# Kernel tuning notes

Hardware: AMD Instinct MI355X
Metric: run time of the kernel (lower is better)

## Reference

```python
import jax, jax.numpy as jnp
import numpy as np

N_NODES = 50000


def setup_inputs() -> dict:
    key = jax.random.key(0)
    ks = jax.random.split(key, 9)
    x = jax.random.normal(ks[0], (N_NODES, 32), dtype=jnp.float32)
    pos = jax.random.normal(ks[1], (N_NODES, 3), dtype=jnp.float32)
    edge_index = jax.random.randint(ks[2], (2, 1600000), 0, N_NODES, dtype=jnp.int64)
    W1 = jax.random.normal(ks[3], (35, 64), dtype=jnp.float32) * 0.1
    b1 = jnp.zeros((64,), dtype=jnp.float32)
    W2 = jax.random.normal(ks[4], (64, 64), dtype=jnp.float32) * 0.1
    b2 = jnp.zeros((64,), dtype=jnp.float32)
    Wg = jax.random.normal(ks[5], (64, 128), dtype=jnp.float32) * 0.1
    bg = jnp.zeros((128,), dtype=jnp.float32)
    return {"x": x, "pos": pos, "edge_index": edge_index,
            "W1": W1, "b1": b1, "W2": W2, "b2": b2, "Wg": Wg, "bg": bg}


def reference(x, pos, edge_index, W1, b1, W2, b2, Wg, bg):
    N = x.shape[0]
    # add_self_loops=True: append (i, i) edges
    self_idx = jnp.arange(N, dtype=edge_index.dtype)
    src = jnp.concatenate([edge_index[0], self_idx])  # message source j
    dst = jnp.concatenate([edge_index[1], self_idx])  # aggregation target i
    # message: concat(x_j, pos_j - pos_i) -> local_nn (Lin+ReLU x2)
    msg = jnp.concatenate([x[src], pos[src] - pos[dst]], axis=-1)  # [E+N, 35]
    h = jax.nn.relu(msg @ W1 + b1)  # [E+N, 64]
    h = jax.nn.relu(h @ W2 + b2)    # [E+N, 64]
    # max aggregation per destination node (self loops guarantee nonempty segments)
    agg = jax.ops.segment_max(h, dst, num_segments=N)  # [N, 64]
    # global_nn: Linear
    return agg @ Wg + bg  # [N, 128]
```

## Files before the change

kernel.cpp:

```cpp
#include <hip/hip_runtime.h>

#define N_NODES 50000
#define N_EDGES 1600000
#define N_TOTAL (N_EDGES + N_NODES)
#define F_IN    32
#define HID     64
#define F_OUT   128
#define G       32
#define NB      1563
#define NBIN    392
#define CAP1_MAX 5120
#define OVF_CAP 16384
#define W1WIN   4096
#define NNODEBLK 196

#define OFF_QBF   0
#define OFF_CUR1  (N_NODES * 32)
#define OFF_OVFC  (OFF_CUR1 + NBIN * 16)
#define OFF_CELLB (OFF_OVFC + 16)
#define OFF_CELLC (OFF_CELLB + NB)
#define OFF_OVF   (OFF_CELLC + NB + 2)
#define OFF_BIN   (OFF_OVF + OVF_CAP)
#define NCLR      (NBIN * 16 + 16)

typedef __attribute__((ext_vector_type(2))) _Float16 h2f;
typedef __attribute__((ext_vector_type(8))) _Float16 half8;
typedef __attribute__((ext_vector_type(4))) float v4f;

__device__ __forceinline__ unsigned f2h2(float a, float b) {
    h2f v;
    v.x = (_Float16)a; v.y = (_Float16)b;
    return __builtin_bit_cast(unsigned, v);
}

__device__ __forceinline__ unsigned hsubmax0(unsigned a, unsigned b) {
    h2f x = __builtin_bit_cast(h2f, a) - __builtin_bit_cast(h2f, b);
    h2f z = {(_Float16)0.f, (_Float16)0.f};
    x = __builtin_elementwise_max(x, z);
    return __builtin_bit_cast(unsigned, x);
}

__device__ __forceinline__ float h2lo(unsigned u) { return (float)__builtin_bit_cast(h2f, u).x; }
__device__ __forceinline__ float h2hi(unsigned u) { return (float)__builtin_bit_cast(h2f, u).y; }
__device__ __forceinline__ float f16r(float x)    { return (float)(_Float16)x; }

#define WAVE_FENCE() do { asm volatile("s_waitcnt lgkmcnt(0)" ::: "memory"); \
                          __builtin_amdgcn_sched_barrier(0); } while (0)

__global__ __launch_bounds__(256) void zero_kernel(unsigned* __restrict__ clr)
{
    const int i = blockIdx.x * 256 + threadIdx.x;
    if (i < NCLR) clr[i] = 0u;
}

__global__ __launch_bounds__(1024) void bin_kernel(
    const int* __restrict__ ei, unsigned* __restrict__ cur1,
    unsigned* __restrict__ bin1, unsigned* __restrict__ ovfc,
    unsigned* __restrict__ ovf, int cap1)
{
    __shared__ unsigned stage[W1WIN];
    __shared__ unsigned hist[NBIN], startp[NBIN + 1], gbase[NBIN];
    __shared__ unsigned wpart[16];

    const int t = threadIdx.x;
    const int wbase = blockIdx.x * W1WIN;

    for (int i = t; i < NBIN; i += 1024) hist[i] = 0u;
    __syncthreads();

    unsigned ev[4]; int bv[4]; unsigned rv[4]; bool val[4];
    #pragma unroll
    for (int k = 0; k < 4; ++k) {
        const int idx = wbase + k * 1024 + t;
        val[k] = idx < N_TOTAL;
        if (val[k]) {
            int s, d;
            if (idx < N_EDGES) { s = ei[idx]; d = ei[N_EDGES + idx]; }
            else               { s = d = idx - N_EDGES; }
            ev[k] = ((unsigned)d << 16) | (unsigned)s;
            bv[k] = d >> 7;
            rv[k] = atomicAdd(&hist[bv[k]], 1u);
        }
    }
    __syncthreads();

    unsigned hv = 0;
    if (t < NBIN) hv = hist[t];
    unsigned v = hv;
    #pragma unroll
    for (int o = 1; o < 64; o <<= 1) {
        const unsigned u = __shfl_up(v, o, 64);
        if ((t & 63) >= o) v += u;
    }
    if ((t & 63) == 63) wpart[t >> 6] = v;
    __syncthreads();
    if (t == 0) {
        unsigned r = 0;
        #pragma unroll
        for (int i = 0; i < 16; ++i) { const unsigned c2 = wpart[i]; wpart[i] = r; r += c2; }
        startp[NBIN] = r;
    }
    __syncthreads();
    if (t < NBIN) startp[t] = (v - hv) + wpart[t >> 6];
    if (t < NBIN && hv) gbase[t] = atomicAdd(&cur1[t * 16], hv);
    __syncthreads();

    #pragma unroll
    for (int k = 0; k < 4; ++k)
        if (val[k]) stage[startp[bv[k]] + rv[k]] = ev[k];
    __syncthreads();

    const unsigned total = startp[NBIN];
    for (unsigned i = t; i < total; i += 1024u) {
        const unsigned e = stage[i];
        const unsigned b = e >> 23;
        const unsigned gp = gbase[b] + (i - startp[b]);
        if (gp < (unsigned)cap1) bin1[b * (unsigned)cap1 + gp] = e;
        else {
            const unsigned qo = atomicAdd(ovfc, 1u);
            if (qo < OVF_CAP) ovf[qo] = e;
        }
    }
}

__global__ __launch_bounds__(1024) void refine_pre_kernel(
    unsigned* __restrict__ bin1, const unsigned* __restrict__ cur1,
    unsigned* __restrict__ cellbase, unsigned* __restrict__ cellcnt, int cap1,
    const float* __restrict__ x, const float* __restrict__ pos,
    const float* __restrict__ W1, const float* __restrict__ b1,
    unsigned* __restrict__ qbf)
{
    __shared__ unsigned ebuf[CAP1_MAX];
    __shared__ unsigned ebuf2[CAP1_MAX];
    __shared__ unsigned cnt32[4 * 32];
    __shared__ unsigned startp[5];
    __shared__ unsigned ssum;
    __shared__ float    w1s[35 * HID + HID];

    const int t = threadIdx.x;

    if (blockIdx.x >= NBIN) {
        for (int i = t; i < 35 * HID; i += 1024) w1s[i] = W1[i];
        if (t < HID) w1s[35 * HID + t] = b1[t];
        __syncthreads();

        const int n = (blockIdx.x - NBIN) * 256 + (t >> 2);
        const int sub = t & 3;
        const int lane = t & 63;
        if (n >= N_NODES) return;

        const float4* x4 = (const float4*)(x + (long long)n * F_IN);
        const float4 xa = x4[sub * 2], xb = x4[sub * 2 + 1];
        const float xv[8] = {xa.x, xa.y, xa.z, xa.w, xb.x, xb.y, xb.z, xb.w};

        float acc[16];
        #pragma unroll
        for (int k = 0; k < 16; ++k) acc[k] = w1s[35 * HID + sub * 16 + k];

        #pragma unroll
        for (int c = 0; c < F_IN; ++c) {
            const float xm = __shfl(xv[c & 7], (lane & 60) | (c >> 3), 64);
            #pragma unroll
            for (int k = 0; k < 16; ++k)
                acc[k] = fmaf(xm, w1s[c * HID + sub * 16 + k], acc[k]);
        }
        #pragma unroll
        for (int a = 0; a < 3; ++a) {
            const float pp = pos[n * 3 + a];
            #pragma unroll
            for (int k = 0; k < 16; ++k)
                acc[k] = fmaf(pp, w1s[(F_IN + a) * HID + sub * 16 + k], acc[k]);
        }

        uint4* o4 = (uint4*)(qbf + (unsigned)n * 32u + (unsigned)sub * 8u);
        o4[0] = make_uint4(f2h2(acc[0], acc[1]),  f2h2(acc[2], acc[3]),
                           f2h2(acc[4], acc[5]),  f2h2(acc[6], acc[7]));
        o4[1] = make_uint4(f2h2(acc[8], acc[9]),  f2h2(acc[10], acc[11]),
                           f2h2(acc[12], acc[13]), f2h2(acc[14], acc[15]));
        return;
    }

    const int bb = blockIdx.x;
    const unsigned n1 = min(cur1[bb * 16], (unsigned)cap1);
    const unsigned base1 = (unsigned)bb * (unsigned)cap1;
    const int rep = t & 31, lane = t & 63;

    if (t < 128) cnt32[t] = 0u;
    __syncthreads();

    for (unsigned i = t; i < n1; i += 1024u) {
        const unsigned e = bin1[base1 + i];
        ebuf[i] = e;
        atomicAdd(&cnt32[(((e >> 21) & 3u) << 5) + rep], 1u);
    }
    __syncthreads();

    unsigned ow = 0;
    if (t < 128) ow = cnt32[t];
    unsigned v = ow;
    #pragma unroll
    for (int o = 1; o < 64; o <<= 1) {
        const unsigned u = __shfl_up(v, o, 64);
        if (lane >= o) v += u;
    }
    if (t == 63) ssum = v;
    __syncthreads();
    if (t >= 64 && t < 128) v += ssum;
    if (t < 128) {
        cnt32[t] = v - ow;
        if ((t & 31) == 0) startp[t >> 5] = v - ow;
    }
    if (t == 0) startp[4] = n1;
    __syncthreads();

    if (t < 4) {
        const int cell = bb * 4 + t;
        if (cell < NB) {
            cellbase[cell] = base1 + startp[t];
            cellcnt[cell]  = startp[t + 1] - startp[t];
        }
    }

    for (unsigned i = t; i < n1; i += 1024u) {
        const unsigned e = ebuf[i];
        const unsigned p = atomicAdd(&cnt32[(((e >> 21) & 3u) << 5) + rep], 1u);
        ebuf2[p] = (((e >> 16) & 31u) << 16) | (e & 0xFFFFu);
    }
    __syncthreads();
    for (unsigned i = t; i < n1; i += 1024u) bin1[base1 + i] = ebuf2[i];
}

__global__ __launch_bounds__(256, 4) void gather_kernel(
    const unsigned* __restrict__ qbf,
    const float* __restrict__ pos,
    const unsigned* __restrict__ cellbase,
    const unsigned* __restrict__ cellcnt,
    const unsigned* __restrict__ bkt,
    const float* __restrict__ W1p,
    const float* __restrict__ W2, const float* __restrict__ b2,
    float* __restrict__ out)
{
    __shared__ unsigned aggs[(G + 1) * HID];
    __shared__ unsigned rlds[G * 32];
    __shared__ unsigned ast[4][64 * 16];

    const int t = threadIdx.x, lane = t & 63, w = t >> 6;
    const int q = lane >> 4, m15 = lane & 15;
    const int b = blockIdx.x;
    const unsigned cnt  = cellcnt[b];
    const unsigned base = cellbase[b];

    for (int i = t; i < (G + 1) * HID; i += 256) aggs[i] = 0u;
    for (int i = t; i < G * 32; i += 256) {
        const int dl = i >> 5, k2 = i & 31;
        const int node = b * G + dl;
        float v0 = 0.f, v1 = 0.f;
        if (node < N_NODES) {
            #pragma unroll
            for (int a = 0; a < 3; ++a) {
                const float pp = pos[node * 3 + a];
                v0 = fmaf(pp, W1p[a * HID + 2 * k2], v0);
                v1 = fmaf(pp, W1p[a * HID + 2 * k2 + 1], v1);
            }
        }
        rlds[(dl << 5) + ((((k2 >> 2) ^ (dl & 7)) << 2) | (k2 & 3))] = f2h2(v0, v1);
    }

    half8 bfr[2][2][2];
    #pragma unroll
    for (int h = 0; h < 2; ++h)
        #pragma unroll
        for (int ntl = 0; ntl < 2; ++ntl) {
            const int nn = (2 * h + ntl) * 16 + m15;
            #pragma unroll
            for (int ks = 0; ks < 2; ++ks) {
                half8 vv;
                #pragma unroll
                for (int j = 0; j < 4; ++j) {
                    const int ku = (ks * 4 + q) * 4 + j;
                    vv[2 * j]     = (_Float16)W2[(2 * ku) * HID + nn];
                    vv[2 * j + 1] = (_Float16)W2[(2 * ku + 1) * HID + nn];
                }
                bfr[h][ntl][ks] = vv;
            }
        }
    float b2v[4];
    #pragma unroll
    for (int nt = 0; nt < 4; ++nt) b2v[nt] = b2[nt * 16 + m15];
    __syncthreads();

    unsigned* aw = ast[w];
    const int axw = ((lane >> 1) & 3) << 2;
    const int axr = ((m15 >> 1) & 3) << 2;
    const unsigned nit = (cnt + 255u) >> 8;

    #pragma unroll 1
    for (unsigned it = 0; it < nit; ++it) {
        const unsigned off = it * 256u + (unsigned)w * 64u;
        const unsigned rem = (off < cnt) ? min(64u, cnt - off) : 0u;
        const unsigned f = off + (unsigned)lane;
        unsigned pent = 0u;
        if (f < cnt) pent = bkt[base + f];
        const int s = (int)(pent & 0xFFFFu), dl = (int)(pent >> 16);

        const uint4* qr = (const uint4*)(qbf + (unsigned)s * 32u);
        const int rbase = dl << 5, rx = dl & 7;

        half8 a0[4], a1[4];

        uint4 qva[4];
        #pragma unroll
        for (int i = 0; i < 4; ++i) qva[i] = qr[i];

        uint4 hh0[4];
        #pragma unroll
        for (int j4 = 0; j4 < 4; ++j4) {
            const uint4 r4 = *(const uint4*)(rlds + rbase + ((j4 ^ rx) << 2));
            hh0[j4].x = hsubmax0(qva[j4].x, r4.x);
            hh0[j4].y = hsubmax0(qva[j4].y, r4.y);
            hh0[j4].z = hsubmax0(qva[j4].z, r4.z);
            hh0[j4].w = hsubmax0(qva[j4].w, r4.w);
        }
        uint4 qvb[4];
        #pragma unroll
        for (int i = 0; i < 4; ++i) qvb[i] = qr[i + 4];

        #pragma unroll
        for (int j4 = 0; j4 < 4; ++j4)
            *(uint4*)(aw + (lane << 4) + ((j4 << 2) ^ axw)) = hh0[j4];
        WAVE_FENCE();
        #pragma unroll
        for (int mt = 0; mt < 4; ++mt)
            a0[mt] = *(const half8*)(
                aw + ((mt * 16 + m15) << 4) + ((q << 2) ^ axr));
        WAVE_FENCE();

        #pragma unroll
        for (int j4 = 0; j4 < 4; ++j4) {
            const uint4 r4 = *(const uint4*)(
                rlds + rbase + (((4 + j4) ^ rx) << 2));
            uint4 hh;
            hh.x = hsubmax0(qvb[j4].x, r4.x);
            hh.y = hsubmax0(qvb[j4].y, r4.y);
            hh.z = hsubmax0(qvb[j4].z, r4.z);
            hh.w = hsubmax0(qvb[j4].w, r4.w);
            *(uint4*)(aw + (lane << 4) + ((j4 << 2) ^ axw)) = hh;
        }
        WAVE_FENCE();
        #pragma unroll
        for (int mt = 0; mt < 4; ++mt)
            a1[mt] = *(const half8*)(
                aw + ((mt * 16 + m15) << 4) + ((q << 2) ^ axr));
        WAVE_FENCE();

        #pragma unroll
        for (int h = 0; h < 2; ++h) {
            v4f c[4][2];
            #pragma unroll
            for (int mt = 0; mt < 4; ++mt)
                #pragma unroll
                for (int ntl = 0; ntl < 2; ++ntl) {
                    const float bb2 = b2v[2 * h + ntl];
                    c[mt][ntl] = (v4f){bb2, bb2, bb2, bb2};
                }
            #pragma unroll
            for (int mt = 0; mt < 4; ++mt)
                #pragma unroll
                for (int ntl = 0; ntl < 2; ++ntl) {
                    c[mt][ntl] = __builtin_amdgcn_mfma_f32_16x16x32_f16(
                        a0[mt], bfr[h][ntl][0], c[mt][ntl], 0, 0, 0);
                    c[mt][ntl] = __builtin_amdgcn_mfma_f32_16x16x32_f16(
                        a1[mt], bfr[h][ntl][1], c[mt][ntl], 0, 0, 0);
                }
            #pragma unroll
            for (int mt = 0; mt < 4; ++mt)
                #pragma unroll
                for (int r = 0; r < 4; ++r) {
                    const int er = mt * 16 + q * 4 + r;
                    const int dv = __shfl(dl, er, 64);
                    const int dle = ((unsigned)er < rem) ? dv : G;
                    const int ab = (dle << 6) + m15;
                    #pragma unroll
                    for (int ntl = 0; ntl < 2; ++ntl) {
                        const float hv = fmaxf(c[mt][ntl][r], 0.f);
                        atomicMax(&aggs[ab + (2 * h + ntl) * 16],
                                  __float_as_uint(hv));
                    }
                }
        }
    }

    __syncthreads();
    for (int i = t; i < G * HID; i += 256) {
        const int row = i >> 6, ch = i & 63, n = b * G + row;
        if (n < N_NODES)
            out[(long long)n * F_OUT + HID + ch] = __uint_as_float(aggs[i]);
    }
}

__global__ __launch_bounds__(64) void ovf_kernel(
    const unsigned* __restrict__ qbf, const float* __restrict__ pos,
    const unsigned* __restrict__ ovfc, const unsigned* __restrict__ ovf,
    const float* __restrict__ W1p, const float* __restrict__ W2,
    const float* __restrict__ b2, unsigned* __restrict__ aggbits)
{
    const unsigned n = min(*ovfc, (unsigned)OVF_CAP);
    for (unsigned i = blockIdx.x * 64 + threadIdx.x; i < n; i += gridDim.x * 64) {
        const unsigned p = ovf[i];
        const int s = (int)(p & 0xFFFFu), d = (int)(p >> 16);
        float h1[HID];
        #pragma unroll 1
        for (int k = 0; k < HID; ++k) {
            const unsigned u = qbf[s * 32 + (k >> 1)];
            const float qp = (k & 1) ? h2hi(u) : h2lo(u);
            float r = 0.f;
            #pragma unroll 1
            for (int a = 0; a < 3; ++a) r = fmaf(pos[d * 3 + a], W1p[a * HID + k], r);
            h1[k] = fmaxf(f16r(qp - f16r(r)), 0.f);
        }
        unsigned* ap = aggbits + (long long)d * F_OUT + HID;
        #pragma unroll 1
        for (int k = 0; k < HID; ++k) {
            float a2 = b2[k];
            #pragma unroll 1
            for (int j = 0; j < HID; ++j)
                a2 = fmaf(h1[j], f16r(W2[j * HID + k]), a2);
            a2 = fmaxf(a2, 0.f);
            atomicMax(ap + k, __float_as_uint(a2));
        }
    }
}

__global__ __launch_bounds__(256) void out_gemm_kernel(
    float* __restrict__ out,
    const float* __restrict__ Wg,
    const float* __restrict__ bg)
{
    const int lane = threadIdx.x & 63;
    const int wave = blockIdx.x * (blockDim.x >> 6) + (threadIdx.x >> 6);
    const int nwav = gridDim.x * (blockDim.x >> 6);

    float w1r[HID], w2r[HID];
    #pragma unroll
    for (int j = 0; j < HID; ++j) {
        w1r[j] = Wg[j * F_OUT + lane];
        w2r[j] = Wg[j * F_OUT + 64 + lane];
    }
    const float bga = bg[lane];
    const float bgb = bg[64 + lane];

    for (int n = wave; n < N_NODES; n += nwav) {
        float* row = out + (long long)n * F_OUT;
        const float a = row[64 + lane];
        float y1 = bga, y2 = bgb;
        #pragma unroll
        for (int j = 0; j < HID; ++j) {
            const float aj = __shfl(a, j, 64);
            y1 = fmaf(aj, w1r[j], y1);
            y2 = fmaf(aj, w2r[j], y2);
        }
        row[lane]      = y1;
        row[64 + lane] = y2;
    }
}

extern "C" void kernel_launch(void* const* d_in, const int* in_sizes, int n_in,
                              void* d_out, int out_size, void* d_ws, size_t ws_size,
                              hipStream_t stream) {
    const float* x   = (const float*)d_in[0];
    const float* pos = (const float*)d_in[1];
    const int*   ei  = (const int*)d_in[2];
    const float* W1  = (const float*)d_in[3];
    const float* b1  = (const float*)d_in[4];
    const float* W2  = (const float*)d_in[5];
    const float* b2  = (const float*)d_in[6];
    const float* Wg  = (const float*)d_in[7];
    const float* bg  = (const float*)d_in[8];
    float* out = (float*)d_out;

    unsigned* ws    = (unsigned*)d_ws;
    unsigned* qbf   = ws + OFF_QBF;
    unsigned* cur1  = ws + OFF_CUR1;
    unsigned* ovfc  = ws + OFF_OVFC;
    unsigned* cellb = ws + OFF_CELLB;
    unsigned* cellc = ws + OFF_CELLC;
    unsigned* ovf   = ws + OFF_OVF;
    unsigned* bin1  = ws + OFF_BIN;

    long long avail = (long long)(ws_size / 4) - OFF_BIN;
    int cap1 = (int)(avail / NBIN);
    if (cap1 > CAP1_MAX) cap1 = CAP1_MAX;
    if (cap1 < 2048) cap1 = 2048;

    zero_kernel<<<(NCLR + 255) / 256, 256, 0, stream>>>(cur1);
    bin_kernel<<<(N_TOTAL + W1WIN - 1) / W1WIN, 1024, 0, stream>>>(
        ei, cur1, bin1, ovfc, ovf, cap1);
    refine_pre_kernel<<<NBIN + NNODEBLK, 1024, 0, stream>>>(
        bin1, cur1, cellb, cellc, cap1, x, pos, W1, b1, qbf);
    gather_kernel<<<NB, 256, 0, stream>>>(
        qbf, pos, cellb, cellc, bin1, W1 + F_IN * HID, W2, b2, out);
    ovf_kernel<<<32, 64, 0, stream>>>(
        qbf, pos, ovfc, ovf, W1 + F_IN * HID, W2, b2, (unsigned*)out);
    out_gemm_kernel<<<512, 256, 0, stream>>>(out, Wg, bg);
}
```

Measured before the change: 212.1 us.

## Bin edges directly into 32-node cells and drop the refine pass

```diff
diff --git a/kernel.cpp b/kernel.cpp
--- a/kernel.cpp
+++ b/kernel.cpp
@@ -8,20 +8,19 @@
 #define F_OUT   128
 #define G       32
 #define NB      1563
-#define NBIN    392
-#define CAP1_MAX 5120
+#define CAP1_MAX 1408
 #define OVF_CAP 16384
 #define W1WIN   4096
+#define NBINBLK  403
 #define NNODEBLK 196
+#define NPAIR   782
 
 #define OFF_QBF   0
 #define OFF_CUR1  (N_NODES * 32)
-#define OFF_OVFC  (OFF_CUR1 + NBIN * 16)
-#define OFF_CELLB (OFF_OVFC + 16)
-#define OFF_CELLC (OFF_CELLB + NB)
-#define OFF_OVF   (OFF_CELLC + NB + 2)
+#define OFF_OVFC  (OFF_CUR1 + NB * 16)
+#define OFF_OVF   (OFF_OVFC + 16)
 #define OFF_BIN   (OFF_OVF + OVF_CAP)
-#define NCLR      (NBIN * 16 + 16)
+#define NCLR      (NB * 16 + 16)
 
 typedef __attribute__((ext_vector_type(2))) _Float16 h2f;
 typedef __attribute__((ext_vector_type(8))) _Float16 half8;
@@ -53,19 +52,66 @@
     if (i < NCLR) clr[i] = 0u;
 }
 
-__global__ __launch_bounds__(1024) void bin_kernel(
-    const int* __restrict__ ei, unsigned* __restrict__ cur1,
-    unsigned* __restrict__ bin1, unsigned* __restrict__ ovfc,
-    unsigned* __restrict__ ovf, int cap1)
+__global__ __launch_bounds__(1024) void bin_pre_kernel(
+    const int* __restrict__ ei,
+    unsigned* __restrict__ cur1, unsigned* __restrict__ bin1,
+    unsigned* __restrict__ ovfc, unsigned* __restrict__ ovf, int cap1,
+    const float* __restrict__ x, const float* __restrict__ pos,
+    const float* __restrict__ W1, const float* __restrict__ b1,
+    unsigned* __restrict__ qbf)
 {
     __shared__ unsigned stage[W1WIN];
-    __shared__ unsigned hist[NBIN], startp[NBIN + 1], gbase[NBIN];
+    __shared__ unsigned hist[NB + 1];
+    __shared__ unsigned startp[NB + 1];
+    __shared__ unsigned gbase[NB];
     __shared__ unsigned wpart[16];
-
-    const int t = threadIdx.x;
+    __shared__ float    w1s[35 * HID + HID];
+
+    const int t = threadIdx.x, lane = t & 63;
+
+    if (blockIdx.x >= NBINBLK) {
+        for (int i = t; i < 35 * HID; i += 1024) w1s[i] = W1[i];
+        if (t < HID) w1s[35 * HID + t] = b1[t];
+        __syncthreads();
+
+        const int n = (blockIdx.x - NBINBLK) * 256 + (t >> 2);
+        const int sub = t & 3;
+        if (n >= N_NODES) return;
+
+        const float4* x4 = (const float4*)(x + (long long)n * F_IN);
+        const float4 xa = x4[sub * 2], xb = x4[sub * 2 + 1];
+        const float xv[8] = {xa.x, xa.y, xa.z, xa.w, xb.x, xb.y, xb.z, xb.w};
+
+        float acc[16];
+        #pragma unroll
+        for (int k = 0; k < 16; ++k) acc[k] = w1s[35 * HID + sub * 16 + k];
+
+        #pragma unroll
+        for (int c = 0; c < F_IN; ++c) {
+            const float xm = __shfl(xv[c & 7], (lane & 60) | (c >> 3), 64);
+            #pragma unroll
+            for (int k = 0; k < 16; ++k)
+                acc[k] = fmaf(xm, w1s[c * HID + sub * 16 + k], acc[k]);
+        }
+        #pragma unroll
+        for (int a = 0; a < 3; ++a) {
+            const float pp = pos[n * 3 + a];
+            #pragma unroll
+            for (int k = 0; k < 16; ++k)
+                acc[k] = fmaf(pp, w1s[(F_IN + a) * HID + sub * 16 + k], acc[k]);
+        }
+
+        uint4* o4 = (uint4*)(qbf + (unsigned)n * 32u + (unsigned)sub * 8u);
+        o4[0] = make_uint4(f2h2(acc[0], acc[1]),  f2h2(acc[2], acc[3]),
+                           f2h2(acc[4], acc[5]),  f2h2(acc[6], acc[7]));
+        o4[1] = make_uint4(f2h2(acc[8], acc[9]),  f2h2(acc[10], acc[11]),
+                           f2h2(acc[12], acc[13]), f2h2(acc[14], acc[15]));
+        return;
+    }
+
     const int wbase = blockIdx.x * W1WIN;
 
-    for (int i = t; i < NBIN; i += 1024) hist[i] = 0u;
+    for (int i = t; i < NB + 1; i += 1024) hist[i] = 0u;
     __syncthreads();
 
     unsigned ev[4]; int bv[4]; unsigned rv[4]; bool val[4];
@@ -78,31 +124,36 @@
             if (idx < N_EDGES) { s = ei[idx]; d = ei[N_EDGES + idx]; }
             else               { s = d = idx - N_EDGES; }
             ev[k] = ((unsigned)d << 16) | (unsigned)s;
-            bv[k] = d >> 7;
+            bv[k] = d >> 5;
             rv[k] = atomicAdd(&hist[bv[k]], 1u);
         }
     }
     __syncthreads();
 
-    unsigned hv = 0;
-    if (t < NBIN) hv = hist[t];
-    unsigned v = hv;
+    unsigned h0 = 0, hpair = 0;
+    if (t < NPAIR) { h0 = hist[2 * t]; hpair = h0 + hist[2 * t + 1]; }
+    unsigned v = hpair;
     #pragma unroll
     for (int o = 1; o < 64; o <<= 1) {
         const unsigned u = __shfl_up(v, o, 64);
-        if ((t & 63) >= o) v += u;
-    }
-    if ((t & 63) == 63) wpart[t >> 6] = v;
+        if (lane >= o) v += u;
+    }
+    if (lane == 63) wpart[t >> 6] = v;
     __syncthreads();
     if (t == 0) {
         unsigned r = 0;
         #pragma unroll
         for (int i = 0; i < 16; ++i) { const unsigned c2 = wpart[i]; wpart[i] = r; r += c2; }
-        startp[NBIN] = r;
-    }
-    __syncthreads();
-    if (t < NBIN) startp[t] = (v - hv) + wpart[t >> 6];
-    if (t < NBIN && hv) gbase[t] = atomicAdd(&cur1[t * 16], hv);
+        startp[NB] = r;
+    }
+    __syncthreads();
+    if (t < NPAIR) {
+        const unsigned bse = (v - hpair) + wpart[t >> 6];
+        startp[2 * t]     = bse;
+        startp[2 * t + 1] = bse + h0;
+    }
+    for (int i = t; i < NB; i += 1024)
+        if (hist[i]) gbase[i] = atomicAdd(&cur1[i * 16], hist[i]);
     __syncthreads();
 
     #pragma unroll
@@ -110,10 +161,10 @@
         if (val[k]) stage[startp[bv[k]] + rv[k]] = ev[k];
     __syncthreads();
 
-    const unsigned total = startp[NBIN];
+    const unsigned total = startp[NB];
     for (unsigned i = t; i < total; i += 1024u) {
         const unsigned e = stage[i];
-        const unsigned b = e >> 23;
+        const unsigned b = e >> 21;
         const unsigned gp = gbase[b] + (i - startp[b]);
         if (gp < (unsigned)cap1) bin1[b * (unsigned)cap1 + gp] = e;
         else {
@@ -123,119 +174,12 @@
     }
 }
 
-__global__ __launch_bounds__(1024) void refine_pre_kernel(
-    unsigned* __restrict__ bin1, const unsigned* __restrict__ cur1,
-    unsigned* __restrict__ cellbase, unsigned* __restrict__ cellcnt, int cap1,
-    const float* __restrict__ x, const float* __restrict__ pos,
-    const float* __restrict__ W1, const float* __restrict__ b1,
-    unsigned* __restrict__ qbf)
-{
-    __shared__ unsigned ebuf[CAP1_MAX];
-    __shared__ unsigned ebuf2[CAP1_MAX];
-    __shared__ unsigned cnt32[4 * 32];
-    __shared__ unsigned startp[5];
-    __shared__ unsigned ssum;
-    __shared__ float    w1s[35 * HID + HID];
-
-    const int t = threadIdx.x;
-
-    if (blockIdx.x >= NBIN) {
-        for (int i = t; i < 35 * HID; i += 1024) w1s[i] = W1[i];
-        if (t < HID) w1s[35 * HID + t] = b1[t];
-        __syncthreads();
-
-        const int n = (blockIdx.x - NBIN) * 256 + (t >> 2);
-        const int sub = t & 3;
-        const int lane = t & 63;
-        if (n >= N_NODES) return;
-
-        const float4* x4 = (const float4*)(x + (long long)n * F_IN);
-        const float4 xa = x4[sub * 2], xb = x4[sub * 2 + 1];
-        const float xv[8] = {xa.x, xa.y, xa.z, xa.w, xb.x, xb.y, xb.z, xb.w};
-
-        float acc[16];
-        #pragma unroll
-        for (int k = 0; k < 16; ++k) acc[k] = w1s[35 * HID + sub * 16 + k];
-
-        #pragma unroll
-        for (int c = 0; c < F_IN; ++c) {
-            const float xm = __shfl(xv[c & 7], (lane & 60) | (c >> 3), 64);
-            #pragma unroll
-            for (int k = 0; k < 16; ++k)
-                acc[k] = fmaf(xm, w1s[c * HID + sub * 16 + k], acc[k]);
-        }
-        #pragma unroll
-        for (int a = 0; a < 3; ++a) {
-            const float pp = pos[n * 3 + a];
-            #pragma unroll
-            for (int k = 0; k < 16; ++k)
-                acc[k] = fmaf(pp, w1s[(F_IN + a) * HID + sub * 16 + k], acc[k]);
-        }
-
-        uint4* o4 = (uint4*)(qbf + (unsigned)n * 32u + (unsigned)sub * 8u);
-        o4[0] = make_uint4(f2h2(acc[0], acc[1]),  f2h2(acc[2], acc[3]),
-                           f2h2(acc[4], acc[5]),  f2h2(acc[6], acc[7]));
-        o4[1] = make_uint4(f2h2(acc[8], acc[9]),  f2h2(acc[10], acc[11]),
-                           f2h2(acc[12], acc[13]), f2h2(acc[14], acc[15]));
-        return;
-    }
-
-    const int bb = blockIdx.x;
-    const unsigned n1 = min(cur1[bb * 16], (unsigned)cap1);
-    const unsigned base1 = (unsigned)bb * (unsigned)cap1;
-    const int rep = t & 31, lane = t & 63;
-
-    if (t < 128) cnt32[t] = 0u;
-    __syncthreads();
-
-    for (unsigned i = t; i < n1; i += 1024u) {
-        const unsigned e = bin1[base1 + i];
-        ebuf[i] = e;
-        atomicAdd(&cnt32[(((e >> 21) & 3u) << 5) + rep], 1u);
-    }
-    __syncthreads();
-
-    unsigned ow = 0;
-    if (t < 128) ow = cnt32[t];
-    unsigned v = ow;
-    #pragma unroll
-    for (int o = 1; o < 64; o <<= 1) {
-        const unsigned u = __shfl_up(v, o, 64);
-        if (lane >= o) v += u;
-    }
-    if (t == 63) ssum = v;
-    __syncthreads();
-    if (t >= 64 && t < 128) v += ssum;
-    if (t < 128) {
-        cnt32[t] = v - ow;
-        if ((t & 31) == 0) startp[t >> 5] = v - ow;
-    }
-    if (t == 0) startp[4] = n1;
-    __syncthreads();
-
-    if (t < 4) {
-        const int cell = bb * 4 + t;
-        if (cell < NB) {
-            cellbase[cell] = base1 + startp[t];
-            cellcnt[cell]  = startp[t + 1] - startp[t];
-        }
-    }
-
-    for (unsigned i = t; i < n1; i += 1024u) {
-        const unsigned e = ebuf[i];
-        const unsigned p = atomicAdd(&cnt32[(((e >> 21) & 3u) << 5) + rep], 1u);
-        ebuf2[p] = (((e >> 16) & 31u) << 16) | (e & 0xFFFFu);
-    }
-    __syncthreads();
-    for (unsigned i = t; i < n1; i += 1024u) bin1[base1 + i] = ebuf2[i];
-}
-
 __global__ __launch_bounds__(256, 4) void gather_kernel(
     const unsigned* __restrict__ qbf,
     const float* __restrict__ pos,
-    const unsigned* __restrict__ cellbase,
-    const unsigned* __restrict__ cellcnt,
+    const unsigned* __restrict__ cur1,
     const unsigned* __restrict__ bkt,
+    int cap1,
     const float* __restrict__ W1p,
     const float* __restrict__ W2, const float* __restrict__ b2,
     float* __restrict__ out)
@@ -247,8 +191,8 @@
     const int t = threadIdx.x, lane = t & 63, w = t >> 6;
     const int q = lane >> 4, m15 = lane & 15;
     const int b = blockIdx.x;
-    const unsigned cnt  = cellcnt[b];
-    const unsigned base = cellbase[b];
+    const unsigned cnt  = min(cur1[b * 16], (unsigned)cap1);
+    const unsigned base = (unsigned)b * (unsigned)cap1;
 
     for (int i = t; i < (G + 1) * HID; i += 256) aggs[i] = 0u;
     for (int i = t; i < G * 32; i += 256) {
@@ -301,7 +245,7 @@
         const unsigned f = off + (unsigned)lane;
         unsigned pent = 0u;
         if (f < cnt) pent = bkt[base + f];
-        const int s = (int)(pent & 0xFFFFu), dl = (int)(pent >> 16);
+        const int s = (int)(pent & 0xFFFFu), dl = (int)((pent >> 16) & 31u);
 
         const uint4* qr = (const uint4*)(qbf + (unsigned)s * 32u);
         const int rbase = dl << 5, rx = dl & 7;
@@ -482,23 +426,19 @@
     unsigned* qbf   = ws + OFF_QBF;
     unsigned* cur1  = ws + OFF_CUR1;
     unsigned* ovfc  = ws + OFF_OVFC;
-    unsigned* cellb = ws + OFF_CELLB;
-    unsigned* cellc = ws + OFF_CELLC;
     unsigned* ovf   = ws + OFF_OVF;
     unsigned* bin1  = ws + OFF_BIN;
 
     long long avail = (long long)(ws_size / 4) - OFF_BIN;
-    int cap1 = (int)(avail / NBIN);
+    int cap1 = (int)(avail / NB);
     if (cap1 > CAP1_MAX) cap1 = CAP1_MAX;
-    if (cap1 < 2048) cap1 = 2048;
+    if (cap1 < 1152) cap1 = 1152;
 
     zero_kernel<<<(NCLR + 255) / 256, 256, 0, stream>>>(cur1);
-    bin_kernel<<<(N_TOTAL + W1WIN - 1) / W1WIN, 1024, 0, stream>>>(
-        ei, cur1, bin1, ovfc, ovf, cap1);
-    refine_pre_kernel<<<NBIN + NNODEBLK, 1024, 0, stream>>>(
-        bin1, cur1, cellb, cellc, cap1, x, pos, W1, b1, qbf);
+    bin_pre_kernel<<<NBINBLK + NNODEBLK, 1024, 0, stream>>>(
+        ei, cur1, bin1, ovfc, ovf, cap1, x, pos, W1, b1, qbf);
     gather_kernel<<<NB, 256, 0, stream>>>(
-        qbf, pos, cellb, cellc, bin1, W1 + F_IN * HID, W2, b2, out);
+        qbf, pos, cur1, bin1, cap1, W1 + F_IN * HID, W2, b2, out);
     ovf_kernel<<<32, 64, 0, stream>>>(
         qbf, pos, ovfc, ovf, W1 + F_IN * HID, W2, b2, (unsigned*)out);
     out_gemm_kernel<<<512, 256, 0, stream>>>(out, Wg, bg);
```

After: 220.0 us. +3.7%, slower.

## Fuse overflow handling and output GEMM into gather kernel epilogue

Applied to the files above, without the earlier changes.

```diff
diff --git a/kernel.cpp b/kernel.cpp
--- a/kernel.cpp
+++ b/kernel.cpp
@@ -40,10 +40,6 @@
     return __builtin_bit_cast(unsigned, x);
 }
 
-__device__ __forceinline__ float h2lo(unsigned u) { return (float)__builtin_bit_cast(h2f, u).x; }
-__device__ __forceinline__ float h2hi(unsigned u) { return (float)__builtin_bit_cast(h2f, u).y; }
-__device__ __forceinline__ float f16r(float x)    { return (float)(_Float16)x; }
-
 #define WAVE_FENCE() do { asm volatile("s_waitcnt lgkmcnt(0)" ::: "memory"); \
                           __builtin_amdgcn_sched_barrier(0); } while (0)
 
@@ -236,8 +232,10 @@
     const unsigned* __restrict__ cellbase,
     const unsigned* __restrict__ cellcnt,
     const unsigned* __restrict__ bkt,
+    const unsigned* __restrict__ ovfc, const unsigned* __restrict__ ovf,
     const float* __restrict__ W1p,
     const float* __restrict__ W2, const float* __restrict__ b2,
+    const float* __restrict__ Wg, const float* __restrict__ bg,
     float* __restrict__ out)
 {
     __shared__ unsigned aggs[(G + 1) * HID];
@@ -249,6 +247,8 @@
     const int b = blockIdx.x;
     const unsigned cnt  = cellcnt[b];
     const unsigned base = cellbase[b];
+    const unsigned no   = min(*ovfc, (unsigned)OVF_CAP);
+    const unsigned tot  = cnt + no;
 
     for (int i = t; i < (G + 1) * HID; i += 256) aggs[i] = 0u;
     for (int i = t; i < G * 32; i += 256) {
@@ -292,16 +292,22 @@
     unsigned* aw = ast[w];
     const int axw = ((lane >> 1) & 3) << 2;
     const int axr = ((m15 >> 1) & 3) << 2;
-    const unsigned nit = (cnt + 255u) >> 8;
+    const unsigned nit = (tot + 255u) >> 8;
 
     #pragma unroll 1
     for (unsigned it = 0; it < nit; ++it) {
         const unsigned off = it * 256u + (unsigned)w * 64u;
-        const unsigned rem = (off < cnt) ? min(64u, cnt - off) : 0u;
         const unsigned f = off + (unsigned)lane;
-        unsigned pent = 0u;
-        if (f < cnt) pent = bkt[base + f];
-        const int s = (int)(pent & 0xFFFFu), dl = (int)(pent >> 16);
+        int s = 0, dle_lane = G;
+        if (f < cnt) {
+            const unsigned p2 = bkt[base + f];
+            s = (int)(p2 & 0xFFFFu); dle_lane = (int)(p2 >> 16);
+        } else if (f < tot) {
+            const unsigned p2 = ovf[f - cnt];
+            s = (int)(p2 & 0xFFFFu);
+            if ((p2 >> 21) == (unsigned)b) dle_lane = (int)((p2 >> 16) & 31u);
+        }
+        const int dl = (dle_lane < G) ? dle_lane : 0;
 
         const uint4* qr = (const uint4*)(qbf + (unsigned)s * 32u);
         const int rbase = dl << 5, rx = dl & 7;
@@ -377,9 +383,8 @@
                 #pragma unroll
                 for (int r = 0; r < 4; ++r) {
                     const int er = mt * 16 + q * 4 + r;
-                    const int dv = __shfl(dl, er, 64);
-                    const int dle = ((unsigned)er < rem) ? dv : G;
-                    const int ab = (dle << 6) + m15;
+                    const int dv = __shfl(dle_lane, er, 64);
+                    const int ab = (dv << 6) + m15;
                     #pragma unroll
                     for (int ntl = 0; ntl < 2; ++ntl) {
                         const float hv = fmaxf(c[mt][ntl][r], 0.f);
@@ -391,76 +396,50 @@
     }
 
     __syncthreads();
-    for (int i = t; i < G * HID; i += 256) {
-        const int row = i >> 6, ch = i & 63, n = b * G + row;
-        if (n < N_NODES)
-            out[(long long)n * F_OUT + HID + ch] = __uint_as_float(aggs[i]);
-    }
-}
-
-__global__ __launch_bounds__(64) void ovf_kernel(
-    const unsigned* __restrict__ qbf, const float* __restrict__ pos,
-    const unsigned* __restrict__ ovfc, const unsigned* __restrict__ ovf,
-    const float* __restrict__ W1p, const float* __restrict__ W2,
-    const float* __restrict__ b2, unsigned* __restrict__ aggbits)
-{
-    const unsigned n = min(*ovfc, (unsigned)OVF_CAP);
-    for (unsigned i = blockIdx.x * 64 + threadIdx.x; i < n; i += gridDim.x * 64) {
-        const unsigned p = ovf[i];
-        const int s = (int)(p & 0xFFFFu), d = (int)(p >> 16);
-        float h1[HID];
-        #pragma unroll 1
-        for (int k = 0; k < HID; ++k) {
-            const unsigned u = qbf[s * 32 + (k >> 1)];
-            const float qp = (k & 1) ? h2hi(u) : h2lo(u);
-            float r = 0.f;
-            #pragma unroll 1
-            for (int a = 0; a < 3; ++a) r = fmaf(pos[d * 3 + a], W1p[a * HID + k], r);
-            h1[k] = fmaxf(f16r(qp - f16r(r)), 0.f);
-        }
-        unsigned* ap = aggbits + (long long)d * F_OUT + HID;
-        #pragma unroll 1
-        for (int k = 0; k < HID; ++k) {
-            float a2 = b2[k];
-            #pragma unroll 1
-            for (int j = 0; j < HID; ++j)
-                a2 = fmaf(h1[j], f16r(W2[j * HID + k]), a2);
-            a2 = fmaxf(a2, 0.f);
-            atomicMax(ap + k, __float_as_uint(a2));
-        }
-    }
-}
-
-__global__ __launch_bounds__(256) void out_gemm_kernel(
-    float* __restrict__ out,
-    const float* __restrict__ Wg,
-    const float* __restrict__ bg)
-{
-    const int lane = threadIdx.x & 63;
-    const int wave = blockIdx.x * (blockDim.x >> 6) + (threadIdx.x >> 6);
-    const int nwav = gridDim.x * (blockDim.x >> 6);
-
-    float w1r[HID], w2r[HID];
-    #pragma unroll
-    for (int j = 0; j < HID; ++j) {
-        w1r[j] = Wg[j * F_OUT + lane];
-        w2r[j] = Wg[j * F_OUT + 64 + lane];
-    }
-    const float bga = bg[lane];
-    const float bgb = bg[64 + lane];
-
-    for (int n = wave; n < N_NODES; n += nwav) {
-        float* row = out + (long long)n * F_OUT;
-        const float a = row[64 + lane];
-        float y1 = bga, y2 = bgb;
-        #pragma unroll
-        for (int j = 0; j < HID; ++j) {
-            const float aj = __shfl(a, j, 64);
-            y1 = fmaf(aj, w1r[j], y1);
-            y2 = fmaf(aj, w2r[j], y2);
-        }
-        row[lane]      = y1;
-        row[64 + lane] = y2;
+    unsigned* wg16 = &ast[0][0];
+    for (int i = t; i < 128 * 32; i += 256) {
+        const int nn = i >> 5, ku = i & 31;
+        wg16[(nn << 5) + ((((ku >> 2) ^ (nn & 7)) << 2) | (ku & 3))] =
+            f2h2(Wg[(2 * ku) * F_OUT + nn], Wg[(2 * ku + 1) * F_OUT + nn]);
+    }
+    __syncthreads();
+
+    half8 af[2][2];
+    #pragma unroll
+    for (int mt2 = 0; mt2 < 2; ++mt2)
+        #pragma unroll
+        for (int ks = 0; ks < 2; ++ks) {
+            const unsigned* ap = aggs + (mt2 * 16 + m15) * 64 + ks * 32 + q * 8;
+            const uint4 u0 = *(const uint4*)ap;
+            const uint4 u1 = *(const uint4*)(ap + 4);
+            uint4 pk;
+            pk.x = f2h2(__uint_as_float(u0.x), __uint_as_float(u0.y));
+            pk.y = f2h2(__uint_as_float(u0.z), __uint_as_float(u0.w));
+            pk.z = f2h2(__uint_as_float(u1.x), __uint_as_float(u1.y));
+            pk.w = f2h2(__uint_as_float(u1.z), __uint_as_float(u1.w));
+            af[mt2][ks] = __builtin_bit_cast(half8, pk);
+        }
+
+    #pragma unroll
+    for (int ntl = 0; ntl < 2; ++ntl) {
+        const int nn = w * 32 + ntl * 16 + m15;
+        const float bgv = bg[nn];
+        half8 bf[2];
+        #pragma unroll
+        for (int ks = 0; ks < 2; ++ks)
+            bf[ks] = *(const half8*)(
+                wg16 + (nn << 5) + ((((ks * 4 + q) ^ (nn & 7)) << 2)));
+        #pragma unroll
+        for (int mt2 = 0; mt2 < 2; ++mt2) {
+            v4f c = (v4f){bgv, bgv, bgv, bgv};
+            c = __builtin_amdgcn_mfma_f32_16x16x32_f16(af[mt2][0], bf[0], c, 0, 0, 0);
+            c = __builtin_amdgcn_mfma_f32_16x16x32_f16(af[mt2][1], bf[1], c, 0, 0, 0);
+            #pragma unroll
+            for (int r = 0; r < 4; ++r) {
+                const int n = b * G + mt2 * 16 + q * 4 + r;
+                if (n < N_NODES) out[(long long)n * F_OUT + nn] = c[r];
+            }
+        }
     }
 }
 
@@ -498,8 +477,6 @@
     refine_pre_kernel<<<NBIN + NNODEBLK, 1024, 0, stream>>>(
         bin1, cur1, cellb, cellc, cap1, x, pos, W1, b1, qbf);
     gather_kernel<<<NB, 256, 0, stream>>>(
-        qbf, pos, cellb, cellc, bin1, W1 + F_IN * HID, W2, b2, out);
-    ovf_kernel<<<32, 64, 0, stream>>>(
-        qbf, pos, ovfc, ovf, W1 + F_IN * HID, W2, b2, (unsigned*)out);
-    out_gemm_kernel<<<512, 256, 0, stream>>>(out, Wg, bg);
-}
+        qbf, pos, cellb, cellc, bin1, ovfc, ovf,
+        W1 + F_IN * HID, W2, b2, Wg, bg, out);
+}
```

Measured after the change: 186.5 us, median of 2. -12.1%, faster.
